# Performance work log

Measured on AMD Instinct MI355X. Metric: run time of the kernel, lower is better.

The kernel has to match this reference:

```python
import jax, jax.numpy as jnp
import numpy as np
import math


def setup_inputs() -> dict:
    key = jax.random.key(0)
    ks = jax.random.split(key, 6)
    B, C, H, W = 4, 384, 64, 64
    nd = 12
    d = C // nd  # 32 = projected channel width
    return {
        "x": jax.random.normal(ks[0], (B, C, H, W), jnp.float32),
        "xe": jax.random.normal(ks[1], (B, C, H, W), jnp.float32),
        "Wq": jax.random.normal(ks[2], (d, C), jnp.float32) * 0.02,      # 1x1 conv C -> d, no bias
        "Wkv": jax.random.normal(ks[3], (2 * d, C), jnp.float32) * 0.02,  # 1x1 conv C -> 2d, no bias
        "Wout": jax.random.normal(ks[4], (C, d, 3, 3), jnp.float32) * 0.02,  # 3x3 conv d -> C
        "bout": jnp.zeros((C,), jnp.float32),
        "n_div": 12,
    }


def reference(x, xe, Wq, Wkv, Wout, bout, n_div):
    B, C, H, W = x.shape
    Y, X = xe.shape[-2], xe.shape[-1]
    n_head = 1
    hd = C // (n_head * n_div)  # head_dim
    # 1x1 conv projections as einsums
    q = jnp.einsum('dc,bchw->bdhw', Wq, x).reshape(B, n_head, hd, H, W)
    kv = jnp.einsum('dc,bchw->bdhw', Wkv, xe).reshape(B, n_head, 2 * hd, Y, X)
    k, v = kv[:, :, :hd], kv[:, :, hd:]
    # full pairwise spatial attention scores [B, n_head, H, W, Y, X]
    scale = 1.0 / math.sqrt(C // n_div)
    attn = jnp.einsum('bnchw,bncyx->bnhwyx', q, k) * scale
    attn = jax.nn.softmax(attn.reshape(B, n_head, H, W, Y * X), axis=-1)
    attn = attn.reshape(B, n_head, H, W, Y, X)
    out = jnp.einsum('bnhwyx,bncyx->bnchw', attn, v).reshape(B, C // n_div, H, W)
    # 3x3 conv with padding 1, plus bias, then residual
    out = jax.lax.conv_general_dilated(
        out, Wout, window_strides=(1, 1), padding='SAME',
        dimension_numbers=('NCHW', 'OIHW', 'NCHW'))
    out = out + bout[None, :, None, None]
    return out + x
```

## Files before the change

kernel.cpp:

```cpp
#include <hip/hip_runtime.h>
#include <hip/hip_bf16.h>
#include <math.h>

#define B_   4
#define C_   384
#define HD_  32
#define P_   4096
#define PADP 4356
#define QSC_ 0.2550889266f

typedef __attribute__((ext_vector_type(4))) float f32x4;
typedef __attribute__((ext_vector_type(8))) short short8;

static __device__ inline unsigned cvt_pk(float lo, float hi) {
    unsigned r;
    asm("v_cvt_pk_bf16_f32 %0, %1, %2" : "=v"(r) : "v"(lo), "v"(hi));
    return r;
}
static __device__ inline float exp2a(float x) {
    float r;
    asm("v_exp_f32 %0, %1" : "=v"(r) : "v"(x));
    return r;
}
static __device__ inline short bf16_bits(float a) {
    __hip_bfloat16 x = __float2bfloat16(a);
    return *reinterpret_cast<short*>(&x);
}

__global__ void repack_kernel(const float* __restrict__ Wq,
                              const float* __restrict__ Wkv,
                              const float* __restrict__ Wout,
                              short* __restrict__ Wball,
                              short* __restrict__ Wbc,
                              unsigned* __restrict__ aoT32) {
    int idx = blockIdx.x * 256 + threadIdx.x;
    if (idx < B_ * 260 * 16) {
        int j = idx & 15;
        int p = (idx >> 4) % 260;
        int b = idx / (260 * 16);
        int hh, ww;
        if (p < 66)       { hh = 0;  ww = p; }
        else if (p < 132) { hh = 65; ww = p - 66; }
        else { int i = p - 132; hh = 1 + (i >> 1); ww = (i & 1) * 65; }
        aoT32[((size_t)b * PADP + hh * 66 + ww) * 16 + j] = 0;
    }
    if (idx < 96 * C_) {
        int r = idx / C_, c = idx % C_;
        float v = (r < 32) ? Wq[r * C_ + c] * QSC_ : Wkv[(r - 32) * C_ + c];
        Wball[idx] = bf16_bits(v);
    }
    int j = idx - 96 * C_;
    if (j >= 0 && j < 9 * 384 * 32) {
        int ci = j & 31;
        int co = (j >> 5) % 384;
        int kk = j / (384 * 32);
        int ky = kk / 3, kx = kk % 3;
        Wbc[j] = bf16_bits(Wout[((co * 32 + ci) * 3 + ky) * 3 + kx]);
    }
}

__global__ __launch_bounds__(768)
void proj_kernel(const float* __restrict__ x, const float* __restrict__ xe,
                 const short* __restrict__ Wball,
                 short* __restrict__ qT, short* __restrict__ kT,
                 short* __restrict__ vT) {
    int b = blockIdx.y;
    int p0 = blockIdx.x << 5;
    int t = threadIdx.x, w = t >> 6, l = t & 63, lq = l & 15, h = l >> 4;
    int mt = w >> 1, pg = w & 1;
    int p = p0 + pg * 16 + lq;
    const float* in = (mt < 2) ? x : xe;
    const float* xb = in + (size_t)b * C_ * P_ + p;
    const short* Ap = Wball + (size_t)(mt * 16 + lq) * C_ + h * 8;
    f32x4 acc = {0.f, 0.f, 0.f, 0.f};
    for (int ks = 0; ks < 12; ++ks) {
        float xv[8];
        #pragma unroll
        for (int jj = 0; jj < 8; ++jj)
            xv[jj] = xb[(size_t)(ks * 32 + h * 8 + jj) * P_];
        unsigned u[4];
        #pragma unroll
        for (int jj = 0; jj < 4; ++jj) u[jj] = cvt_pk(xv[2 * jj], xv[2 * jj + 1]);
        short8 bf;
        __builtin_memcpy(&bf, u, 16);
        short8 af = *(const short8*)(Ap + ks * 32);
        acc = __builtin_amdgcn_mfma_f32_16x16x32_bf16(af, bf, acc, 0, 0, 0);
    }
    if (mt < 4) {
        short* dst = (mt < 2) ? qT : kT;
        int d = (mt & 1) * 16 + h * 4;
        uint2 u;
        u.x = cvt_pk(acc[0], acc[1]);
        u.y = cvt_pk(acc[2], acc[3]);
        *(uint2*)(dst + ((size_t)b * P_ + p) * HD_ + d) = u;
    } else {
        int d = (mt - 4) * 16 + h * 4;
        #pragma unroll
        for (int r = 0; r < 4; ++r)
            vT[((size_t)b * HD_ + d + r) * P_ + p] = bf16_bits(acc[r]);
    }
}

__global__ __launch_bounds__(256, 4)
void attn_mfma_kernel(const short* __restrict__ qT,
                      const short* __restrict__ kT,
                      const short* __restrict__ vT,
                      short* __restrict__ aoT) {
    __shared__ unsigned p_lds[4][512];
    __shared__ float o_lds[4][32][16];
    __shared__ float l_lds[4][16];

    int blk = blockIdx.x;
    int b = blk >> 8;
    int q0 = (blk & 255) << 4;
    int t = threadIdx.x, w = t >> 6, l = t & 63, lq = l & 15, h = l >> 4;

    const short* qTb = qT + ((size_t)b * P_ + q0) * HD_;
    const short* kTb = kT + (size_t)b * P_ * HD_;
    const short* vb  = vT + (size_t)b * HD_ * P_;

    short8 qf = *(const short8*)(qTb + lq * HD_ + h * 8);

    f32x4 o0 = {0.f, 0.f, 0.f, 0.f}, o1 = {0.f, 0.f, 0.f, 0.f};
    float lsum = 0.f;
    unsigned* myp = &p_lds[w][0];
    int swz = (lq & 7) << 4;

    int key_base = w * 1024;
    short8 kf[4], vf[4];
    {
        const short* kp = kTb + (size_t)(key_base + lq) * HD_ + h * 8;
        #pragma unroll
        for (int tt = 0; tt < 4; ++tt) kf[tt] = *(const short8*)(kp + tt * 16 * HD_);
        const short* vp = vb + (size_t)lq * P_ + key_base + h * 8;
        vf[0] = *(const short8*)(vp);
        vf[1] = *(const short8*)(vp + 32);
        vf[2] = *(const short8*)(vp + 16 * P_);
        vf[3] = *(const short8*)(vp + 16 * P_ + 32);
    }

    for (int kt = 0; kt < 16; ++kt) {
        short8 nk[4], nv[4];
        if (kt < 15) {
            int nxt = key_base + (kt + 1) * 64;
            const short* kp = kTb + (size_t)(nxt + lq) * HD_ + h * 8;
            #pragma unroll
            for (int tt = 0; tt < 4; ++tt) nk[tt] = *(const short8*)(kp + tt * 16 * HD_);
            const short* vp = vb + (size_t)lq * P_ + nxt + h * 8;
            nv[0] = *(const short8*)(vp);
            nv[1] = *(const short8*)(vp + 32);
            nv[2] = *(const short8*)(vp + 16 * P_);
            nv[3] = *(const short8*)(vp + 16 * P_ + 32);
        } else {
            #pragma unroll
            for (int tt = 0; tt < 4; ++tt) { nk[tt] = kf[tt]; nv[tt] = vf[tt]; }
        }

        f32x4 st[4];
        __builtin_amdgcn_s_setprio(1);
        #pragma unroll
        for (int tt = 0; tt < 4; ++tt)
            st[tt] = __builtin_amdgcn_mfma_f32_16x16x32_bf16(kf[tt], qf,
                         (f32x4){0.f, 0.f, 0.f, 0.f}, 0, 0, 0);
        __builtin_amdgcn_s_setprio(0);

        float e[16];
        #pragma unroll
        for (int tt = 0; tt < 4; ++tt)
            #pragma unroll
            for (int r = 0; r < 4; ++r) e[tt * 4 + r] = exp2a(st[tt][r]);
        float ls = 0.f;
        #pragma unroll
        for (int i = 0; i < 16; i += 4)
            ls += (e[i] + e[i + 1]) + (e[i + 2] + e[i + 3]);
        lsum += ls;

        #pragma unroll
        for (int tt = 0; tt < 4; ++tt) {
            int u0 = tt * 32 + h * 8;
            myp[(lq * 128 + ((u0 + 0) ^ swz)) >> 2] = cvt_pk(e[tt * 4 + 0], e[tt * 4 + 1]);
            myp[(lq * 128 + ((u0 + 4) ^ swz)) >> 2] = cvt_pk(e[tt * 4 + 2], e[tt * 4 + 3]);
        }
        short8 pb0, pb1;
        __builtin_memcpy(&pb0, (const char*)myp + lq * 128 + ((h * 16 + 0)  ^ swz), 16);
        __builtin_memcpy(&pb1, (const char*)myp + lq * 128 + ((h * 16 + 64) ^ swz), 16);

        __builtin_amdgcn_s_setprio(1);
        o0 = __builtin_amdgcn_mfma_f32_16x16x32_bf16(vf[0], pb0, o0, 0, 0, 0);
        o0 = __builtin_amdgcn_mfma_f32_16x16x32_bf16(vf[1], pb1, o0, 0, 0, 0);
        o1 = __builtin_amdgcn_mfma_f32_16x16x32_bf16(vf[2], pb0, o1, 0, 0, 0);
        o1 = __builtin_amdgcn_mfma_f32_16x16x32_bf16(vf[3], pb1, o1, 0, 0, 0);
        __builtin_amdgcn_s_setprio(0);

        #pragma unroll
        for (int tt = 0; tt < 4; ++tt) { kf[tt] = nk[tt]; vf[tt] = nv[tt]; }
    }

    lsum += __shfl_xor(lsum, 16);
    lsum += __shfl_xor(lsum, 32);

    #pragma unroll
    for (int r = 0; r < 4; ++r) {
        o_lds[w][h * 4 + r][lq]      = o0[r];
        o_lds[w][16 + h * 4 + r][lq] = o1[r];
    }
    if (h == 0) l_lds[w][lq] = lsum;
    __syncthreads();

    {
        int qq = t >> 4;
        int d0 = (t & 15) * 2;
        float denom = l_lds[0][qq] + l_lds[1][qq] + l_lds[2][qq] + l_lds[3][qq];
        float v0 = 0.f, v1 = 0.f;
        #pragma unroll
        for (int ww = 0; ww < 4; ++ww) {
            v0 += o_lds[ww][d0][qq];
            v1 += o_lds[ww][d0 + 1][qq];
        }
        float inv = 1.f / denom;
        int p = q0 + qq;
        int hh = p >> 6, ww2 = p & 63;
        unsigned* dst = (unsigned*)(aoT +
            ((size_t)b * PADP + (hh + 1) * 66 + (ww2 + 1)) * HD_ + d0);
        *dst = cvt_pk(v0 * inv, v1 * inv);
    }
}

__global__ __launch_bounds__(512)
void conv_mfma_kernel(const short* __restrict__ Wbc,
                      const short* __restrict__ aoT,
                      const float* __restrict__ bout,
                      const float* __restrict__ x,
                      float* __restrict__ out) {
    int blk = blockIdx.x;
    int b = blk >> 7;
    int p0 = (blk & 127) << 5;
    int t = threadIdx.x;
    int w = t >> 6, l = t & 63, lq = l & 15, h = l >> 4;
    int co0 = w * 48;

    const short* aob = aoT + (size_t)b * PADP * HD_;
    const short* bptr[2];
    #pragma unroll
    for (int n = 0; n < 2; ++n) {
        int p = p0 + n * 16 + lq;
        int hh = p >> 6, ww = p & 63;
        bptr[n] = aob + (size_t)(hh * 66 + ww) * HD_ + h * 8;
    }
    const short* aptr = Wbc + (size_t)(co0 + lq) * 32 + h * 8;

    f32x4 acc[3][2];
    #pragma unroll
    for (int m = 0; m < 3; ++m)
        #pragma unroll
        for (int n = 0; n < 2; ++n) acc[m][n] = (f32x4){0.f, 0.f, 0.f, 0.f};

    short8 Bf0 = *(const short8*)(bptr[0]);
    short8 Bf1 = *(const short8*)(bptr[1]);
    #pragma unroll
    for (int kk = 0; kk < 9; ++kk) {
        short8 nB0, nB1;
        if (kk < 8) {
            int ky = (kk + 1) / 3, kx = (kk + 1) % 3;
            nB0 = *(const short8*)(bptr[0] + (ky * 66 + kx) * HD_);
            nB1 = *(const short8*)(bptr[1] + (ky * 66 + kx) * HD_);
        } else { nB0 = Bf0; nB1 = Bf1; }
        #pragma unroll
        for (int m = 0; m < 3; ++m) {
            short8 Af = *(const short8*)(aptr + kk * 12288 + m * 512);
            acc[m][0] = __builtin_amdgcn_mfma_f32_16x16x32_bf16(Af, Bf0, acc[m][0], 0, 0, 0);
            acc[m][1] = __builtin_amdgcn_mfma_f32_16x16x32_bf16(Af, Bf1, acc[m][1], 0, 0, 0);
        }
        Bf0 = nB0; Bf1 = nB1;
    }

    #pragma unroll
    for (int m = 0; m < 3; ++m) {
        #pragma unroll
        for (int r = 0; r < 4; ++r) {
            int co = co0 + m * 16 + h * 4 + r;
            float bias = bout[co];
            #pragma unroll
            for (int n = 0; n < 2; ++n) {
                int p = p0 + n * 16 + lq;
                size_t idx = ((size_t)b * C_ + co) * P_ + p;
                out[idx] = acc[m][n][r] + bias + x[idx];
            }
        }
    }
}

extern "C" void kernel_launch(void* const* d_in, const int* in_sizes, int n_in,
                              void* d_out, int out_size, void* d_ws, size_t ws_size,
                              hipStream_t stream) {
    const float* x    = (const float*)d_in[0];
    const float* xe   = (const float*)d_in[1];
    const float* Wq   = (const float*)d_in[2];
    const float* Wkv  = (const float*)d_in[3];
    const float* Wout = (const float*)d_in[4];
    const float* bout = (const float*)d_in[5];
    float* out = (float*)d_out;

    short* qT    = (short*)d_ws;
    short* kT    = qT  + (size_t)B_ * P_ * HD_;
    short* vT    = kT  + (size_t)B_ * P_ * HD_;
    short* aoT   = vT  + (size_t)B_ * P_ * HD_;
    short* Wball = aoT + (size_t)B_ * PADP * HD_;
    short* Wbc   = Wball + 96 * C_;

    repack_kernel<<<576, 256, 0, stream>>>(Wq, Wkv, Wout, Wball, Wbc, (unsigned*)aoT);
    proj_kernel<<<dim3(128, B_), 768, 0, stream>>>(x, xe, Wball, qT, kT, vT);
    attn_mfma_kernel<<<B_ * 256, 256, 0, stream>>>(qT, kT, vT, aoT);
    conv_mfma_kernel<<<B_ * 128, 512, 0, stream>>>(Wbc, aoT, bout, x, out);
}
```

Measured before the change: 89.60 us.

## Process two query tiles per wave to reuse K/V fragments in attention

The attention kernel now gives each block 32 queries and 8 waves instead of 16 queries and 4 waves. Each wave handles 512 keys and runs two 16-query tiles against the same K and V fragments, so each K/V load is reused across twice as many queries. V is now loaded inside the loop instead of being prefetched a step ahead, and the cross-wave reduction of outputs and row sums goes through LDS float atomics into one shared buffer instead of per-wave slots. The cost is more registers per wave, a larger LDS footprint, half as many blocks, and atomic contention when the waves combine results.

```diff
diff --git a/kernel.cpp b/kernel.cpp
--- a/kernel.cpp
+++ b/kernel.cpp
@@ -101,123 +101,131 @@
     }
 }
 
-__global__ __launch_bounds__(256, 4)
+__global__ __launch_bounds__(512, 4)
 void attn_mfma_kernel(const short* __restrict__ qT,
                       const short* __restrict__ kT,
                       const short* __restrict__ vT,
                       short* __restrict__ aoT) {
-    __shared__ unsigned p_lds[4][512];
-    __shared__ float o_lds[4][32][16];
-    __shared__ float l_lds[4][16];
+    __shared__ unsigned p_lds[8][1024];
+    __shared__ float o_sh[32][33];
+    __shared__ float l_sh[32];
 
     int blk = blockIdx.x;
-    int b = blk >> 8;
-    int q0 = (blk & 255) << 4;
+    int b = blk >> 7;
+    int q0 = (blk & 127) << 5;
     int t = threadIdx.x, w = t >> 6, l = t & 63, lq = l & 15, h = l >> 4;
+
+    for (int i = t; i < 32 * 33; i += 512) ((float*)o_sh)[i] = 0.f;
+    if (t < 32) l_sh[t] = 0.f;
 
     const short* qTb = qT + ((size_t)b * P_ + q0) * HD_;
     const short* kTb = kT + (size_t)b * P_ * HD_;
     const short* vb  = vT + (size_t)b * HD_ * P_;
 
-    short8 qf = *(const short8*)(qTb + lq * HD_ + h * 8);
-
-    f32x4 o0 = {0.f, 0.f, 0.f, 0.f}, o1 = {0.f, 0.f, 0.f, 0.f};
-    float lsum = 0.f;
+    short8 qf0 = *(const short8*)(qTb + lq * HD_ + h * 8);
+    short8 qf1 = *(const short8*)(qTb + (16 + lq) * HD_ + h * 8);
+
+    f32x4 o00 = {0.f,0.f,0.f,0.f}, o01 = {0.f,0.f,0.f,0.f};
+    f32x4 o10 = {0.f,0.f,0.f,0.f}, o11 = {0.f,0.f,0.f,0.f};
+    float lsum0 = 0.f, lsum1 = 0.f;
     unsigned* myp = &p_lds[w][0];
     int swz = (lq & 7) << 4;
 
-    int key_base = w * 1024;
-    short8 kf[4], vf[4];
+    int key_base = w * 512;
+    short8 kf[4];
     {
         const short* kp = kTb + (size_t)(key_base + lq) * HD_ + h * 8;
         #pragma unroll
         for (int tt = 0; tt < 4; ++tt) kf[tt] = *(const short8*)(kp + tt * 16 * HD_);
-        const short* vp = vb + (size_t)lq * P_ + key_base + h * 8;
-        vf[0] = *(const short8*)(vp);
-        vf[1] = *(const short8*)(vp + 32);
-        vf[2] = *(const short8*)(vp + 16 * P_);
-        vf[3] = *(const short8*)(vp + 16 * P_ + 32);
-    }
-
-    for (int kt = 0; kt < 16; ++kt) {
-        short8 nk[4], nv[4];
-        if (kt < 15) {
-            int nxt = key_base + (kt + 1) * 64;
-            const short* kp = kTb + (size_t)(nxt + lq) * HD_ + h * 8;
-            #pragma unroll
-            for (int tt = 0; tt < 4; ++tt) nk[tt] = *(const short8*)(kp + tt * 16 * HD_);
-            const short* vp = vb + (size_t)lq * P_ + nxt + h * 8;
-            nv[0] = *(const short8*)(vp);
-            nv[1] = *(const short8*)(vp + 32);
-            nv[2] = *(const short8*)(vp + 16 * P_);
-            nv[3] = *(const short8*)(vp + 16 * P_ + 32);
-        } else {
-            #pragma unroll
-            for (int tt = 0; tt < 4; ++tt) { nk[tt] = kf[tt]; nv[tt] = vf[tt]; }
-        }
-
-        f32x4 st[4];
+    }
+    __syncthreads();
+
+    for (int kt = 0; kt < 8; ++kt) {
+        int key0 = key_base + kt * 64;
+        const short* vp = vb + (size_t)lq * P_ + key0 + h * 8;
+        short8 vf0 = *(const short8*)(vp);
+        short8 vf1 = *(const short8*)(vp + 32);
+        short8 vf2 = *(const short8*)(vp + 16 * P_);
+        short8 vf3 = *(const short8*)(vp + 16 * P_ + 32);
+
+        f32x4 st0[4], st1[4];
         __builtin_amdgcn_s_setprio(1);
         #pragma unroll
-        for (int tt = 0; tt < 4; ++tt)
-            st[tt] = __builtin_amdgcn_mfma_f32_16x16x32_bf16(kf[tt], qf,
-                         (f32x4){0.f, 0.f, 0.f, 0.f}, 0, 0, 0);
+        for (int tt = 0; tt < 4; ++tt) {
+            st0[tt] = __builtin_amdgcn_mfma_f32_16x16x32_bf16(kf[tt], qf0,
+                          (f32x4){0.f,0.f,0.f,0.f}, 0, 0, 0);
+            st1[tt] = __builtin_amdgcn_mfma_f32_16x16x32_bf16(kf[tt], qf1,
+                          (f32x4){0.f,0.f,0.f,0.f}, 0, 0, 0);
+        }
         __builtin_amdgcn_s_setprio(0);
 
-        float e[16];
-        #pragma unroll
-        for (int tt = 0; tt < 4; ++tt)
-            #pragma unroll
-            for (int r = 0; r < 4; ++r) e[tt * 4 + r] = exp2a(st[tt][r]);
-        float ls = 0.f;
-        #pragma unroll
-        for (int i = 0; i < 16; i += 4)
-            ls += (e[i] + e[i + 1]) + (e[i + 2] + e[i + 3]);
-        lsum += ls;
-
-        #pragma unroll
-        for (int tt = 0; tt < 4; ++tt) {
-            int u0 = tt * 32 + h * 8;
-            myp[(lq * 128 + ((u0 + 0) ^ swz)) >> 2] = cvt_pk(e[tt * 4 + 0], e[tt * 4 + 1]);
-            myp[(lq * 128 + ((u0 + 4) ^ swz)) >> 2] = cvt_pk(e[tt * 4 + 2], e[tt * 4 + 3]);
-        }
-        short8 pb0, pb1;
-        __builtin_memcpy(&pb0, (const char*)myp + lq * 128 + ((h * 16 + 0)  ^ swz), 16);
-        __builtin_memcpy(&pb1, (const char*)myp + lq * 128 + ((h * 16 + 64) ^ swz), 16);
+        if (kt < 7) {
+            const short* kp = kTb + (size_t)(key0 + 64 + lq) * HD_ + h * 8;
+            #pragma unroll
+            for (int tt = 0; tt < 4; ++tt) kf[tt] = *(const short8*)(kp + tt * 16 * HD_);
+        }
+
+        #pragma unroll
+        for (int qt = 0; qt < 2; ++qt) {
+            f32x4* st = qt ? st1 : st0;
+            float e[16];
+            #pragma unroll
+            for (int tt = 0; tt < 4; ++tt)
+                #pragma unroll
+                for (int r = 0; r < 4; ++r) e[tt * 4 + r] = exp2a(st[tt][r]);
+            float ls = 0.f;
+            #pragma unroll
+            for (int i = 0; i < 16; i += 4)
+                ls += (e[i] + e[i + 1]) + (e[i + 2] + e[i + 3]);
+            if (qt) lsum1 += ls; else lsum0 += ls;
+            unsigned* row = myp + ((qt * 16 + lq) * 128 >> 2);
+            #pragma unroll
+            for (int tt = 0; tt < 4; ++tt) {
+                int u0 = tt * 32 + h * 8;
+                row[((u0 + 0) ^ swz) >> 2] = cvt_pk(e[tt * 4 + 0], e[tt * 4 + 1]);
+                row[((u0 + 4) ^ swz) >> 2] = cvt_pk(e[tt * 4 + 2], e[tt * 4 + 3]);
+            }
+        }
+
+        short8 pb00, pb01, pb10, pb11;
+        __builtin_memcpy(&pb00, (const char*)myp + lq * 128        + ((h * 16 + 0)  ^ swz), 16);
+        __builtin_memcpy(&pb01, (const char*)myp + lq * 128        + ((h * 16 + 64) ^ swz), 16);
+        __builtin_memcpy(&pb10, (const char*)myp + (16 + lq) * 128 + ((h * 16 + 0)  ^ swz), 16);
+        __builtin_memcpy(&pb11, (const char*)myp + (16 + lq) * 128 + ((h * 16 + 64) ^ swz), 16);
 
         __builtin_amdgcn_s_setprio(1);
-        o0 = __builtin_amdgcn_mfma_f32_16x16x32_bf16(vf[0], pb0, o0, 0, 0, 0);
-        o0 = __builtin_amdgcn_mfma_f32_16x16x32_bf16(vf[1], pb1, o0, 0, 0, 0);
-        o1 = __builtin_amdgcn_mfma_f32_16x16x32_bf16(vf[2], pb0, o1, 0, 0, 0);
-        o1 = __builtin_amdgcn_mfma_f32_16x16x32_bf16(vf[3], pb1, o1, 0, 0, 0);
+        o00 = __builtin_amdgcn_mfma_f32_16x16x32_bf16(vf0, pb00, o00, 0, 0, 0);
+        o00 = __builtin_amdgcn_mfma_f32_16x16x32_bf16(vf1, pb01, o00, 0, 0, 0);
+        o01 = __builtin_amdgcn_mfma_f32_16x16x32_bf16(vf0, pb10, o01, 0, 0, 0);
+        o01 = __builtin_amdgcn_mfma_f32_16x16x32_bf16(vf1, pb11, o01, 0, 0, 0);
+        o10 = __builtin_amdgcn_mfma_f32_16x16x32_bf16(vf2, pb00, o10, 0, 0, 0);
+        o10 = __builtin_amdgcn_mfma_f32_16x16x32_bf16(vf3, pb01, o10, 0, 0, 0);
+        o11 = __builtin_amdgcn_mfma_f32_16x16x32_bf16(vf2, pb10, o11, 0, 0, 0);
+        o11 = __builtin_amdgcn_mfma_f32_16x16x32_bf16(vf3, pb11, o11, 0, 0, 0);
         __builtin_amdgcn_s_setprio(0);
-
-        #pragma unroll
-        for (int tt = 0; tt < 4; ++tt) { kf[tt] = nk[tt]; vf[tt] = nv[tt]; }
-    }
-
-    lsum += __shfl_xor(lsum, 16);
-    lsum += __shfl_xor(lsum, 32);
+    }
+
+    lsum0 += __shfl_xor(lsum0, 16); lsum0 += __shfl_xor(lsum0, 32);
+    lsum1 += __shfl_xor(lsum1, 16); lsum1 += __shfl_xor(lsum1, 32);
 
     #pragma unroll
     for (int r = 0; r < 4; ++r) {
-        o_lds[w][h * 4 + r][lq]      = o0[r];
-        o_lds[w][16 + h * 4 + r][lq] = o1[r];
-    }
-    if (h == 0) l_lds[w][lq] = lsum;
+        atomicAdd(&o_sh[h * 4 + r][lq],           o00[r]);
+        atomicAdd(&o_sh[h * 4 + r][16 + lq],      o01[r]);
+        atomicAdd(&o_sh[16 + h * 4 + r][lq],      o10[r]);
+        atomicAdd(&o_sh[16 + h * 4 + r][16 + lq], o11[r]);
+    }
+    if (h == 0) {
+        atomicAdd(&l_sh[lq],      lsum0);
+        atomicAdd(&l_sh[16 + lq], lsum1);
+    }
     __syncthreads();
 
     {
         int qq = t >> 4;
         int d0 = (t & 15) * 2;
-        float denom = l_lds[0][qq] + l_lds[1][qq] + l_lds[2][qq] + l_lds[3][qq];
-        float v0 = 0.f, v1 = 0.f;
-        #pragma unroll
-        for (int ww = 0; ww < 4; ++ww) {
-            v0 += o_lds[ww][d0][qq];
-            v1 += o_lds[ww][d0 + 1][qq];
-        }
-        float inv = 1.f / denom;
+        float inv = 1.f / l_sh[qq];
+        float v0 = o_sh[d0][qq], v1 = o_sh[d0 + 1][qq];
         int p = q0 + qq;
         int hh = p >> 6, ww2 = p & 63;
         unsigned* dst = (unsigned*)(aoT +
@@ -310,6 +318,6 @@
 
     repack_kernel<<<576, 256, 0, stream>>>(Wq, Wkv, Wout, Wball, Wbc, (unsigned*)aoT);
     proj_kernel<<<dim3(128, B_), 768, 0, stream>>>(x, xe, Wball, qT, kT, vT);
-    attn_mfma_kernel<<<B_ * 256, 256, 0, stream>>>(qT, kT, vT, aoT);
+    attn_mfma_kernel<<<B_ * 128, 512, 0, stream>>>(qT, kT, vT, aoT);
     conv_mfma_kernel<<<B_ * 128, 512, 0, stream>>>(Wbc, aoT, bout, x, out);
 }
```

New measurement: 90.49 us. Within noise of the previous version (+1.0%).
